# Kernel tuning notes

Hardware: AMD Instinct MI355X
Metric: run time of the kernel (lower is better)

The kernel has to match this reference:

```python
import jax, jax.numpy as jnp
import numpy as np

N, E = 5000, 10000          # nodes, edges
F_IN, F_EDGE = 16, 4        # raw node / edge feature dims
H, EH, HID3 = 96, 16, 32    # node hidden, edge hidden, edge-MLP hidden
T, L, C = 5, 10, 3          # Chebyshev order, num DeepGCN layers, num classes
LN_EPS = 1e-5


def setup_inputs() -> dict:
    key = jax.random.key(0)
    ks = jax.random.split(key, 12)
    x = jax.random.normal(ks[0], (N, F_IN), jnp.float32)
    edge_index = jax.random.randint(ks[1], (2, E), 0, N)
    ea = jax.random.uniform(ks[2], (E, F_EDGE), dtype=jnp.float32)
    # first column is an edge-type flag; ~half the edges are 'sequence' edges (type 0)
    etype = jax.random.randint(ks[3], (E,), 0, 2).astype(jnp.float32)
    edge_attr = ea.at[:, 0].set(etype)

    def glorot(k, sh, fan):
        return jax.random.normal(k, sh, jnp.float32) / np.float32(np.sqrt(fan))

    cheb_w = glorot(ks[4], (T, F_IN, H), F_IN)
    cheb_b = jnp.zeros((H,), jnp.float32)
    enc_w = glorot(ks[5], (F_EDGE, EH), F_EDGE)
    enc_b = jnp.zeros((EH,), jnp.float32)
    # per-layer NNConv edge MLP (MapE2NxN): 16 -> 32 -> 96*96
    mlp_w1 = glorot(ks[6], (L, EH, HID3), EH)
    mlp_b1 = jnp.zeros((L, HID3), jnp.float32)
    mlp_w2 = glorot(ks[7], (L, HID3, H * H), HID3) * 0.1  # keep edge-weight magnitudes sane
    mlp_b2 = jnp.zeros((L, H * H), jnp.float32)
    root = glorot(ks[8], (L, H, H), H)
    conv_b = jnp.zeros((L, H), jnp.float32)
    ln_g = jnp.ones((L, H), jnp.float32)
    ln_b = jnp.zeros((L, H), jnp.float32)
    lin_w = glorot(ks[9], (H, C), H)
    lin_b = jnp.zeros((C,), jnp.float32)
    return dict(x=x, edge_index=edge_index, edge_attr=edge_attr,
                cheb_w=cheb_w, cheb_b=cheb_b, enc_w=enc_w, enc_b=enc_b,
                mlp_w1=mlp_w1, mlp_b1=mlp_b1, mlp_w2=mlp_w2, mlp_b2=mlp_b2,
                root=root, conv_b=conv_b, ln_g=ln_g, ln_b=ln_b,
                lin_w=lin_w, lin_b=lin_b)


def _layer_norm(v, g, b):
    mu = jnp.mean(v, axis=-1, keepdims=True)
    var = jnp.mean((v - mu) ** 2, axis=-1, keepdims=True)
    return (v - mu) * jax.lax.rsqrt(var + LN_EPS) * g + b


def _cheb_conv(x, row, col, mask, W, b):
    # symmetric-normalized Laplacian, lambda_max=2 => L_hat = -D^-1/2 A D^-1/2 (diag 0)
    # mask zeroes out non-sequence edges and self loops (PyG removes self loops)
    deg = jax.ops.segment_sum(mask, row, num_segments=N)
    dinv = jnp.where(deg > 0, deg ** -0.5, 0.0)
    w = -dinv[row] * dinv[col] * mask  # [E]
    Lmul = lambda v: jax.ops.segment_sum(w[:, None] * v[row], col, num_segments=N)
    Tx0 = x
    out = Tx0 @ W[0]
    Tx1 = Lmul(x)
    out = out + Tx1 @ W[1]
    for k in range(2, T):
        Tx2 = 2.0 * Lmul(Tx1) - Tx0
        out = out + Tx2 @ W[k]
        Tx0, Tx1 = Tx1, Tx2
    return out + b


def _nnconv(x, row, col, ea, w1, b1, w2, b2, rt, cb):
    # per-edge weight matrix from edge MLP (dropout in eval mode = identity)
    We = ((ea @ w1 + b1) @ w2 + b2).reshape(E, H, H)
    msg = jnp.einsum('eh,eho->eo', x[row], We)          # gather + per-edge GEMM
    agg = jax.ops.segment_sum(msg, col, num_segments=N)  # scatter-add aggregation
    return agg + x @ rt + cb


def reference(x, edge_index, edge_attr, cheb_w, cheb_b, enc_w, enc_b,
              mlp_w1, mlp_b1, mlp_w2, mlp_b2, root, conv_b, ln_g, ln_b,
              lin_w, lin_b):
    row, col = edge_index[0], edge_index[1]
    # sequence edges (edge type 0), excluding self loops, expressed as a weight mask
    seq_mask = ((edge_attr[:, 0] == 0) & (row != col)).astype(x.dtype)
    h = _cheb_conv(x, row, col, seq_mask, cheb_w, cheb_b)          # node encoder
    ea = edge_attr @ enc_w + enc_b                                  # edge encoder
    # layer 0: conv only
    h = _nnconv(h, row, col, ea, mlp_w1[0], mlp_b1[0], mlp_w2[0], mlp_b2[0],
                root[0], conv_b[0])
    # layers 1..L-1: res+ block (norm -> relu -> [dropout=id] -> conv -> +res)
    for i in range(1, L):
        r = h
        v = jax.nn.relu(_layer_norm(h, ln_g[i], ln_b[i]))
        h = _nnconv(v, row, col, ea, mlp_w1[i], mlp_b1[i], mlp_w2[i], mlp_b2[i],
                    root[i], conv_b[i]) + r
    h = jax.nn.relu(_layer_norm(h, ln_g[0], ln_b[0]))  # layers[0].act(layers[0].norm(x))
    return h @ lin_w + lin_b
```

## Files before the change

### kernel.cpp

```cpp
#include <hip/hip_runtime.h>

#define NN 5000
#define EE 10000
#define F_IN 16
#define F_EDGE 4
#define H 96
#define EHD 16
#define HID3 32
#define T_CHEB 5
#define L_LAYERS 10
#define C_OUT 3
#define LN_EPSF 1e-5f
#define KW 576
#define MD 32
#define BM2 16
#define NBT2 313
#define KC_N 36
#define FRAG_PER_LAYER (6 * KC_N * 64)

typedef float float4v __attribute__((ext_vector_type(4)));
typedef _Float16 half2v __attribute__((ext_vector_type(2)));
typedef _Float16 half4v __attribute__((ext_vector_type(4)));
typedef _Float16 half8v __attribute__((ext_vector_type(8)));

#define MFMA16(a, b, c) __builtin_amdgcn_mfma_f32_16x16x16f16((a), (b), (c), 0, 0, 0)

__global__ void k_front(const float* __restrict__ enc_w, const float* __restrict__ enc_b,
                        const float* __restrict__ w1, const float* __restrict__ b1,
                        const float* __restrict__ w2, const float* __restrict__ b2,
                        const float* __restrict__ root,
                        const int* __restrict__ row, const int* __restrict__ col,
                        const float* __restrict__ eattr,
                        _Float16* __restrict__ Mf, float* __restrict__ deg,
                        int* __restrict__ cnt, int* __restrict__ ell_r,
                        float* __restrict__ ell_m, float4* __restrict__ ell_ea) {
    const int tid = blockIdx.x * blockDim.x + threadIdx.x;
    const int NTH = gridDim.x * blockDim.x;
    for (int idx = tid; idx < L_LAYERS * H * H; idx += NTH) {
        int i = idx / (H * H);
        int m = idx % (H * H);
        int h = m / H, o = m % H;
        const float* w2i = w2 + (size_t)i * HID3 * H * H;
        const float* w1i = w1 + i * EHD * HID3;
        float hcol[HID3];
        #pragma unroll
        for (int k2 = 0; k2 < HID3; ++k2) hcol[k2] = w2i[(size_t)k2 * H * H + m];
        float tcol[EHD];
        #pragma unroll
        for (int ke = 0; ke < EHD; ++ke) {
            float s = 0.f;
            #pragma unroll
            for (int k2 = 0; k2 < HID3; ++k2) s += w1i[ke * HID3 + k2] * hcol[k2];
            tcol[ke] = s;
        }
        float vals[6];
        #pragma unroll
        for (int f = 0; f < F_EDGE; ++f) {
            float s = 0.f;
            #pragma unroll
            for (int ke = 0; ke < EHD; ++ke) s += enc_w[f * EHD + ke] * tcol[ke];
            vals[f] = s;
        }
        float c = b2[(size_t)i * H * H + m];
        #pragma unroll
        for (int ke = 0; ke < EHD; ++ke) c += enc_b[ke] * tcol[ke];
        #pragma unroll
        for (int k2 = 0; k2 < HID3; ++k2) c += b1[i * HID3 + k2] * hcol[k2];
        vals[4] = c;
        vals[5] = root[(size_t)i * H * H + m];
        int nt = o >> 4, n15 = o & 15;
        #pragma unroll
        for (int f = 0; f < 6; ++f) {
            int K = f * 96 + h;
            int kc = K >> 4, g2 = (K & 15) >> 2, e2 = K & 3;
            int lane = n15 + 16 * g2;
            Mf[((((size_t)i * 6 + nt) * KC_N + kc) * 64 + lane) * 4 + e2] = (_Float16)vals[f];
        }
    }
    for (int e = tid; e < EE; e += NTH) {
        int r = row[e], c = col[e];
        float4 ea = *(const float4*)(eattr + e * F_EDGE);
        float m = (ea.x == 0.f && r != c) ? 1.f : 0.f;
        if (m != 0.f) atomicAdd(&deg[r], 1.f);
        int slot = atomicAdd(&cnt[c], 1);
        int p = c * MD + slot;
        ell_r[p] = r;
        ell_m[p] = m;
        ell_ea[p] = ea;
    }
}

__global__ void k_chebA(const int* __restrict__ cnt, const int* __restrict__ ell_r,
                        const float* __restrict__ ell_m, const float* __restrict__ deg,
                        const float* __restrict__ x,
                        float* __restrict__ T1, float* __restrict__ T2) {
    int t = blockIdx.x * blockDim.x + threadIdx.x;
    if (t >= NN * 4) return;
    int c = t >> 2, q = t & 3;
    float dc = deg[c];
    float dinvC = dc > 0.f ? rsqrtf(dc) : 0.f;
    int nc = cnt[c];
    const int* rp = ell_r + c * MD;
    const float* mp = ell_m + c * MD;
    float4 acc1 = make_float4(0.f, 0.f, 0.f, 0.f);
    float4 acc2 = make_float4(0.f, 0.f, 0.f, 0.f);
    for (int p = 0; p < nc; ++p) {
        if (mp[p] == 0.f) continue;
        int r = rp[p];
        float dinvR = rsqrtf(deg[r]);
        float4 xr = *(const float4*)(x + (size_t)r * F_IN + q * 4);
        acc1.x = fmaf(dinvR, xr.x, acc1.x); acc1.y = fmaf(dinvR, xr.y, acc1.y);
        acc1.z = fmaf(dinvR, xr.z, acc1.z); acc1.w = fmaf(dinvR, xr.w, acc1.w);
        float4 a = make_float4(0.f, 0.f, 0.f, 0.f);
        int nr = cnt[r];
        const int* rp2 = ell_r + r * MD;
        const float* mp2 = ell_m + r * MD;
        for (int p2 = 0; p2 < nr; ++p2) {
            if (mp2[p2] == 0.f) continue;
            int r2 = rp2[p2];
            float w2v = rsqrtf(deg[r2]);
            float4 x2 = *(const float4*)(x + (size_t)r2 * F_IN + q * 4);
            a.x = fmaf(w2v, x2.x, a.x); a.y = fmaf(w2v, x2.y, a.y);
            a.z = fmaf(w2v, x2.z, a.z); a.w = fmaf(w2v, x2.w, a.w);
        }
        float f1 = -dinvR;
        acc2.x = fmaf(dinvR, f1 * a.x, acc2.x); acc2.y = fmaf(dinvR, f1 * a.y, acc2.y);
        acc2.z = fmaf(dinvR, f1 * a.z, acc2.z); acc2.w = fmaf(dinvR, f1 * a.w, acc2.w);
    }
    float4 xc = *(const float4*)(x + (size_t)c * F_IN + q * 4);
    float f = -dinvC;
    *(float4*)(T1 + (size_t)c * F_IN + q * 4) =
        make_float4(f * acc1.x, f * acc1.y, f * acc1.z, f * acc1.w);
    float f2 = -2.f * dinvC;
    *(float4*)(T2 + (size_t)c * F_IN + q * 4) =
        make_float4(f2 * acc2.x - xc.x, f2 * acc2.y - xc.y,
                    f2 * acc2.z - xc.z, f2 * acc2.w - xc.w);
}

__global__ __launch_bounds__(256) void k_chebB(
        const int* __restrict__ cnt, const int* __restrict__ ell_r,
        const float* __restrict__ ell_m, const float* __restrict__ deg,
        const float* __restrict__ x, const float* __restrict__ T1,
        const float* __restrict__ T2, const float* __restrict__ cheb_w,
        const float* __restrict__ cheb_b, _Float16* __restrict__ vout) {
    __shared__ float wlds[T_CHEB * F_IN][H];
    __shared__ float t34[2][64][F_IN];
    const int n0 = blockIdx.x * 64;
    const int t = threadIdx.x;
    for (int i = t; i < T_CHEB * F_IN * H / 4; i += 256)
        ((float4*)wlds)[i] = ((const float4*)cheb_w)[i];
    {
        int c = n0 + (t >> 2), q = t & 3;
        if (c < NN) {
            float dc = deg[c];
            float dinvC = dc > 0.f ? rsqrtf(dc) : 0.f;
            int nc = cnt[c];
            const int* rp = ell_r + c * MD;
            const float* mp = ell_m + c * MD;
            float4 a3 = make_float4(0.f, 0.f, 0.f, 0.f);
            float4 a4 = make_float4(0.f, 0.f, 0.f, 0.f);
            for (int p = 0; p < nc; ++p) {
                if (mp[p] == 0.f) continue;
                int r = rp[p];
                float dinvR = rsqrtf(deg[r]);
                float4 t2r = *(const float4*)(T2 + (size_t)r * F_IN + q * 4);
                a3.x = fmaf(dinvR, t2r.x, a3.x); a3.y = fmaf(dinvR, t2r.y, a3.y);
                a3.z = fmaf(dinvR, t2r.z, a3.z); a3.w = fmaf(dinvR, t2r.w, a3.w);
                float4 b = make_float4(0.f, 0.f, 0.f, 0.f);
                int nr = cnt[r];
                const int* rp2 = ell_r + r * MD;
                const float* mp2 = ell_m + r * MD;
                for (int p2 = 0; p2 < nr; ++p2) {
                    if (mp2[p2] == 0.f) continue;
                    int r2 = rp2[p2];
                    float w2v = rsqrtf(deg[r2]);
                    float4 t2b = *(const float4*)(T2 + (size_t)r2 * F_IN + q * 4);
                    b.x = fmaf(w2v, t2b.x, b.x); b.y = fmaf(w2v, t2b.y, b.y);
                    b.z = fmaf(w2v, t2b.z, b.z); b.w = fmaf(w2v, t2b.w, b.w);
                }
                float fr = -2.f * dinvR;
                float4 t1r = *(const float4*)(T1 + (size_t)r * F_IN + q * 4);
                float4 t3r = make_float4(fr * b.x - t1r.x, fr * b.y - t1r.y,
                                         fr * b.z - t1r.z, fr * b.w - t1r.w);
                a4.x = fmaf(dinvR, t3r.x, a4.x); a4.y = fmaf(dinvR, t3r.y, a4.y);
                a4.z = fmaf(dinvR, t3r.z, a4.z); a4.w = fmaf(dinvR, t3r.w, a4.w);
            }
            float f3 = -2.f * dinvC;
            float4 t1c = *(const float4*)(T1 + (size_t)c * F_IN + q * 4);
            float4 t2c = *(const float4*)(T2 + (size_t)c * F_IN + q * 4);
            int lr = t >> 2;
            *(float4*)&t34[0][lr][q * 4] =
                make_float4(f3 * a3.x - t1c.x, f3 * a3.y - t1c.y,
                            f3 * a3.z - t1c.z, f3 * a3.w - t1c.w);
            *(float4*)&t34[1][lr][q * 4] =
                make_float4(f3 * a4.x - t2c.x, f3 * a4.y - t2c.y,
                            f3 * a4.z - t2c.z, f3 * a4.w - t2c.w);
        }
    }
    __syncthreads();
    {
        int lr = t >> 2, n = n0 + lr, cseg = t & 3;
        if (n >= NN) return;
        float txv[T_CHEB * F_IN];
        #pragma unroll
        for (int q = 0; q < 4; ++q) {
            *(float4*)(txv + q * 4)      = *(const float4*)(x  + (size_t)n * F_IN + q * 4);
            *(float4*)(txv + 16 + q * 4) = *(const float4*)(T1 + (size_t)n * F_IN + q * 4);
            *(float4*)(txv + 32 + q * 4) = *(const float4*)(T2 + (size_t)n * F_IN + q * 4);
            *(float4*)(txv + 48 + q * 4) = *(const float4*)&t34[0][lr][q * 4];
            *(float4*)(txv + 64 + q * 4) = *(const float4*)&t34[1][lr][q * 4];
        }
        _Float16* vr = vout + (size_t)n * H + cseg * 24;
        #pragma unroll 4
        for (int c = 0; c < 24; ++c) {
            int o = cseg * 24 + c;
            float s = cheb_b[o];
            #pragma unroll
            for (int kf = 0; kf < T_CHEB * F_IN; ++kf)
                s = fmaf(txv[kf], wlds[kf][o], s);
            vr[c] = (_Float16)s;
        }
    }
}

__global__ __launch_bounds__(512) void k_layer(
        const _Float16* __restrict__ vcur, const float* __restrict__ hres,
        const int* __restrict__ cnt, const int* __restrict__ ell_r,
        const float4* __restrict__ ell_ea, const _Float16* __restrict__ MfL,
        const float* __restrict__ cb, const float* __restrict__ lg,
        const float* __restrict__ lb, const float* __restrict__ lin_w,
        const float* __restrict__ lin_b,
        float* __restrict__ hnext, _Float16* __restrict__ vnext,
        float* __restrict__ outp, int isLast) {
    __shared__ __align__(16) _Float16 zs[BM2][584];
    __shared__ float hop[4][BM2][100];
    const int n0 = blockIdx.x * BM2;
    const int t = threadIdx.x;

    if (t < 256) {
        int r = t >> 4, lane16 = t & 15;
        int gn = n0 + r, c0 = lane16 * 6;
        float accf[5][6] = {};
        half2v self0 = (half2v)(_Float16)0.f, self1 = self0, self2 = self0;
        if (gn < NN) {
            const _Float16* sv = vcur + (size_t)gn * H + c0;
            self0 = *(const half2v*)(sv + 0);
            self1 = *(const half2v*)(sv + 2);
            self2 = *(const half2v*)(sv + 4);
            int nc = cnt[gn];
            const int* rp = ell_r + gn * MD;
            const float4* eap = ell_ea + gn * MD;
            for (int p = 0; p < nc; ++p) {
                int r2 = rp[p];
                float4 ea = eap[p];
                const _Float16* vv = vcur + (size_t)r2 * H + c0;
                half2v v0 = *(const half2v*)(vv + 0);
                half2v v1 = *(const half2v*)(vv + 2);
                half2v v2 = *(const half2v*)(vv + 4);
                float vf[6] = {(float)v0[0], (float)v0[1], (float)v1[0],
                               (float)v1[1], (float)v2[0], (float)v2[1]};
                const float cf[4] = {ea.x, ea.y, ea.z, ea.w};
                #pragma unroll
                for (int f = 0; f < 4; ++f)
                    #pragma unroll
                    for (int j = 0; j < 6; ++j)
                        accf[f][j] = fmaf(cf[f], vf[j], accf[f][j]);
                #pragma unroll
                for (int j = 0; j < 6; ++j) accf[4][j] += vf[j];
            }
        }
        #pragma unroll
        for (int f = 0; f < 5; ++f) {
            _Float16* zp = &zs[r][f * 96 + c0];
            *(half2v*)(zp + 0) = half2v{(_Float16)accf[f][0], (_Float16)accf[f][1]};
            *(half2v*)(zp + 2) = half2v{(_Float16)accf[f][2], (_Float16)accf[f][3]};
            *(half2v*)(zp + 4) = half2v{(_Float16)accf[f][4], (_Float16)accf[f][5]};
        }
        _Float16* zp = &zs[r][480 + c0];
        *(half2v*)(zp + 0) = self0;
        *(half2v*)(zp + 2) = self1;
        *(half2v*)(zp + 4) = self2;
    }
    __syncthreads();

    {
        const int wid = t >> 6, l = t & 63;
        const int n15 = l & 15, g = l >> 4;
        const int ntBase = (wid & 1) * 3;
        const int kSeg = wid >> 1;
        const int kcBase = kSeg * 9;
        const half4v* Mf4 = (const half4v*)MfL;
        half4v af[9];
        #pragma unroll
        for (int kk = 0; kk < 9; ++kk)
            af[kk] = *(const half4v*)&zs[n15][(kcBase + kk) * 16 + 4 * g];
        float4v acc3[3] = {};
        #pragma unroll
        for (int j = 0; j < 3; ++j) {
            int nt = ntBase + j;
            const half4v* Bp = Mf4 + ((size_t)nt * KC_N + kcBase) * 64 + l;
            #pragma unroll
            for (int kk = 0; kk < 9; ++kk)
                acc3[j] = MFMA16(af[kk], Bp[kk * 64], acc3[j]);
        }
        #pragma unroll
        for (int j = 0; j < 3; ++j) {
            int cc = (ntBase + j) * 16 + n15;
            #pragma unroll
            for (int e = 0; e < 4; ++e)
                hop[kSeg][4 * g + e][cc] = acc3[j][e];
        }
    }
    __syncthreads();

    if (t < 256) {
        int r = t >> 4, lane16 = t & 15;
        int gn = n0 + r, c0 = lane16 * 6;
        float hv[6];
        #pragma unroll
        for (int j = 0; j < 6; ++j)
            hv[j] = hop[0][r][c0 + j] + hop[1][r][c0 + j]
                  + hop[2][r][c0 + j] + hop[3][r][c0 + j] + cb[c0 + j];
        if (hres && gn < NN) {
            const float* rp = hres + (size_t)gn * H + c0;
            #pragma unroll
            for (int j = 0; j < 6; j += 2) {
                float2 rv = *(const float2*)(rp + j);
                hv[j] += rv.x; hv[j + 1] += rv.y;
            }
        }
        if (!isLast && gn < NN) {
            float* hp = hnext + (size_t)gn * H + c0;
            #pragma unroll
            for (int j = 0; j < 6; j += 2)
                *(float2*)(hp + j) = make_float2(hv[j], hv[j + 1]);
        }
        float s = 0.f;
        #pragma unroll
        for (int j = 0; j < 6; ++j) s += hv[j];
        s += __shfl_xor(s, 1); s += __shfl_xor(s, 2);
        s += __shfl_xor(s, 4); s += __shfl_xor(s, 8);
        float mu = s * (1.0f / H);
        float vvr = 0.f;
        #pragma unroll
        for (int j = 0; j < 6; ++j) { float d = hv[j] - mu; vvr += d * d; }
        vvr += __shfl_xor(vvr, 1); vvr += __shfl_xor(vvr, 2);
        vvr += __shfl_xor(vvr, 4); vvr += __shfl_xor(vvr, 8);
        float is = rsqrtf(vvr * (1.0f / H) + LN_EPSF);
        const float* gp = lg + c0;
        const float* bp = lb + c0;
        float yv[6];
        #pragma unroll
        for (int j = 0; j < 6; ++j)
            yv[j] = fmaxf(fmaf((hv[j] - mu) * is, gp[j], bp[j]), 0.f);
        if (!isLast) {
            if (gn < NN) {
                _Float16* vp = vnext + (size_t)gn * H + c0;
                *(half2v*)(vp + 0) = half2v{(_Float16)yv[0], (_Float16)yv[1]};
                *(half2v*)(vp + 2) = half2v{(_Float16)yv[2], (_Float16)yv[3]};
                *(half2v*)(vp + 4) = half2v{(_Float16)yv[4], (_Float16)yv[5]};
            }
        } else {
            float a0 = 0.f, a1 = 0.f, a2 = 0.f;
            #pragma unroll
            for (int j = 0; j < 6; ++j) {
                int oo = c0 + j;
                a0 = fmaf(yv[j], lin_w[oo * C_OUT + 0], a0);
                a1 = fmaf(yv[j], lin_w[oo * C_OUT + 1], a1);
                a2 = fmaf(yv[j], lin_w[oo * C_OUT + 2], a2);
            }
            a0 += __shfl_xor(a0, 1); a0 += __shfl_xor(a0, 2);
            a0 += __shfl_xor(a0, 4); a0 += __shfl_xor(a0, 8);
            a1 += __shfl_xor(a1, 1); a1 += __shfl_xor(a1, 2);
            a1 += __shfl_xor(a1, 4); a1 += __shfl_xor(a1, 8);
            a2 += __shfl_xor(a2, 1); a2 += __shfl_xor(a2, 2);
            a2 += __shfl_xor(a2, 4); a2 += __shfl_xor(a2, 8);
            if (lane16 == 0 && gn < NN) {
                outp[gn * C_OUT + 0] = a0 + lin_b[0];
                outp[gn * C_OUT + 1] = a1 + lin_b[1];
                outp[gn * C_OUT + 2] = a2 + lin_b[2];
            }
        }
    }
}

extern "C" void kernel_launch(void* const* d_in, const int* in_sizes, int n_in,
                              void* d_out, int out_size, void* d_ws, size_t ws_size,
                              hipStream_t stream) {
    const float* x      = (const float*)d_in[0];
    const int*   row    = (const int*)d_in[1];
    const int*   col    = (const int*)d_in[1] + EE;
    const float* eattr  = (const float*)d_in[2];
    const float* cheb_w = (const float*)d_in[3];
    const float* cheb_b = (const float*)d_in[4];
    const float* enc_w  = (const float*)d_in[5];
    const float* enc_b  = (const float*)d_in[6];
    const float* w1     = (const float*)d_in[7];
    const float* b1     = (const float*)d_in[8];
    const float* w2     = (const float*)d_in[9];
    const float* b2     = (const float*)d_in[10];
    const float* root   = (const float*)d_in[11];
    const float* conv_b = (const float*)d_in[12];
    const float* ln_g   = (const float*)d_in[13];
    const float* ln_b   = (const float*)d_in[14];
    const float* lin_w  = (const float*)d_in[15];
    const float* lin_b  = (const float*)d_in[16];

    char* base = (char*)d_ws;
    size_t off = 0;
    auto alloc = [&](size_t nbytes) {
        char* p = base + off;
        off += (nbytes + 255) / 256 * 256;
        return p;
    };
    float*    deg    = (float*)alloc(NN * 4);
    int*      cnt    = (int*)  alloc(NN * 4);
    size_t    ctl_bytes = off;
    _Float16* Mfrag  = (_Float16*)alloc((size_t)L_LAYERS * FRAG_PER_LAYER * 4 * 2);
    float*    T1     = (float*)alloc((size_t)NN * F_IN * 4);
    float*    T2     = (float*)alloc((size_t)NN * F_IN * 4);
    int*      ell_r  = (int*)  alloc((size_t)NN * MD * 4);
    float*    ell_m  = (float*)alloc((size_t)NN * MD * 4);
    float4*   ell_ea = (float4*)alloc((size_t)NN * MD * 16);
    _Float16* v0     = (_Float16*)alloc((size_t)NN * H * 2);
    _Float16* v1     = (_Float16*)alloc((size_t)NN * H * 2);
    float*    hA     = (float*)alloc((size_t)NN * H * 4);
    float*    hB     = (float*)alloc((size_t)NN * H * 4);
    (void)ws_size; (void)n_in; (void)in_sizes; (void)out_size;

    const int B = 256;
    auto G = [](long n, int b) { return (int)((n + b - 1) / b); };

    (void)hipMemsetAsync(deg, 0, ctl_bytes, stream);
    k_front<<<360, B, 0, stream>>>(enc_w, enc_b, w1, b1, w2, b2, root,
                                   row, col, eattr, Mfrag, deg, cnt, ell_r, ell_m, ell_ea);
    k_chebA<<<G((long)NN * 4, B), B, 0, stream>>>(cnt, ell_r, ell_m, deg, x, T1, T2);
    k_chebB<<<G(NN, 64), B, 0, stream>>>(cnt, ell_r, ell_m, deg, x, T1, T2,
                                         cheb_w, cheb_b, v0);

    _Float16* vbuf[2] = { v0, v1 };
    float*    hbuf[2] = { hA, hB };
    for (int li = 0; li < L_LAYERS; ++li) {
        int isLast = (li == L_LAYERS - 1);
        const _Float16* vcur = vbuf[li & 1];
        _Float16*       vnx  = vbuf[(li + 1) & 1];
        const float*    hres = (li > 0) ? hbuf[(li + 1) & 1] : nullptr;
        float*          hnx  = hbuf[li & 1];
        const float* elg = isLast ? ln_g : ln_g + (li + 1) * H;
        const float* elb = isLast ? ln_b : ln_b + (li + 1) * H;
        k_layer<<<NBT2, 512, 0, stream>>>(
            vcur, hres, cnt, ell_r, ell_ea,
            Mfrag + (size_t)li * FRAG_PER_LAYER * 4,
            conv_b + li * H, elg, elb, lin_w, lin_b,
            hnx, vnx, (float*)d_out, isLast);
    }
}
```

Baseline: 164.6 us.

## Build edge ELL in one block with LDS atomics; prefetch MFMA B fragments early

Edge bucketing and degree counting now run in a dedicated extra block of k_front using shared-memory atomics, and the block writes deg and cnt directly. This removes the separate hipMemsetAsync and the global atomics. In k_layer, each wave loads its B-operand weight fragments into registers at kernel start, so those global loads overlap the neighbor-gather phase instead of sitting behind the barrier. The costs are one block serially handling all 10000 edges, which may lengthen the front kernel, and 27 extra half4 registers per thread in k_layer, which may reduce occupancy.

```diff
diff --git a/kernel.cpp b/kernel.cpp
--- a/kernel.cpp
+++ b/kernel.cpp
@@ -25,17 +25,41 @@
 
 #define MFMA16(a, b, c) __builtin_amdgcn_mfma_f32_16x16x16f16((a), (b), (c), 0, 0, 0)
 
-__global__ void k_front(const float* __restrict__ enc_w, const float* __restrict__ enc_b,
-                        const float* __restrict__ w1, const float* __restrict__ b1,
-                        const float* __restrict__ w2, const float* __restrict__ b2,
-                        const float* __restrict__ root,
-                        const int* __restrict__ row, const int* __restrict__ col,
-                        const float* __restrict__ eattr,
-                        _Float16* __restrict__ Mf, float* __restrict__ deg,
-                        int* __restrict__ cnt, int* __restrict__ ell_r,
-                        float* __restrict__ ell_m, float4* __restrict__ ell_ea) {
-    const int tid = blockIdx.x * blockDim.x + threadIdx.x;
-    const int NTH = gridDim.x * blockDim.x;
+__global__ __launch_bounds__(256) void k_front(
+        const float* __restrict__ enc_w, const float* __restrict__ enc_b,
+        const float* __restrict__ w1, const float* __restrict__ b1,
+        const float* __restrict__ w2, const float* __restrict__ b2,
+        const float* __restrict__ root,
+        const int* __restrict__ row, const int* __restrict__ col,
+        const float* __restrict__ eattr,
+        _Float16* __restrict__ Mf, float* __restrict__ deg,
+        int* __restrict__ cnt, int* __restrict__ ell_r,
+        float* __restrict__ ell_m, float4* __restrict__ ell_ea) {
+    __shared__ int sdeg[NN];
+    __shared__ int scnt[NN];
+    if (blockIdx.x == 0) {
+        for (int i = threadIdx.x; i < NN; i += 256) { sdeg[i] = 0; scnt[i] = 0; }
+        __syncthreads();
+        for (int e = threadIdx.x; e < EE; e += 256) {
+            int r = row[e], c = col[e];
+            float4 ea = *(const float4*)(eattr + e * F_EDGE);
+            float m = (ea.x == 0.f && r != c) ? 1.f : 0.f;
+            if (m != 0.f) atomicAdd(&sdeg[r], 1);
+            int slot = atomicAdd(&scnt[c], 1);
+            int p = c * MD + slot;
+            ell_r[p] = r;
+            ell_m[p] = m;
+            ell_ea[p] = ea;
+        }
+        __syncthreads();
+        for (int i = threadIdx.x; i < NN; i += 256) {
+            deg[i] = (float)sdeg[i];
+            cnt[i] = scnt[i];
+        }
+        return;
+    }
+    const int tid = (blockIdx.x - 1) * 256 + threadIdx.x;
+    const int NTH = (gridDim.x - 1) * 256;
     for (int idx = tid; idx < L_LAYERS * H * H; idx += NTH) {
         int i = idx / (H * H);
         int m = idx % (H * H);
@@ -76,17 +100,6 @@
             int lane = n15 + 16 * g2;
             Mf[((((size_t)i * 6 + nt) * KC_N + kc) * 64 + lane) * 4 + e2] = (_Float16)vals[f];
         }
-    }
-    for (int e = tid; e < EE; e += NTH) {
-        int r = row[e], c = col[e];
-        float4 ea = *(const float4*)(eattr + e * F_EDGE);
-        float m = (ea.x == 0.f && r != c) ? 1.f : 0.f;
-        if (m != 0.f) atomicAdd(&deg[r], 1.f);
-        int slot = atomicAdd(&cnt[c], 1);
-        int p = c * MD + slot;
-        ell_r[p] = r;
-        ell_m[p] = m;
-        ell_ea[p] = ea;
     }
 }
 
@@ -237,6 +250,20 @@
     const int n0 = blockIdx.x * BM2;
     const int t = threadIdx.x;
 
+    const int wid = t >> 6, l = t & 63;
+    const int n15 = l & 15, g = l >> 4;
+    const int ntBase = (wid & 1) * 3;
+    const int kSeg = wid >> 1;
+    const int kcBase = kSeg * 9;
+    const half4v* Mf4 = (const half4v*)MfL;
+    half4v bfr[3][9];
+    #pragma unroll
+    for (int j = 0; j < 3; ++j) {
+        const half4v* Bp = Mf4 + ((size_t)(ntBase + j) * KC_N + kcBase) * 64 + l;
+        #pragma unroll
+        for (int kk = 0; kk < 9; ++kk) bfr[j][kk] = Bp[kk * 64];
+    }
+
     if (t < 256) {
         int r = t >> 4, lane16 = t & 15;
         int gn = n0 + r, c0 = lane16 * 6;
@@ -284,25 +311,16 @@
     __syncthreads();
 
     {
-        const int wid = t >> 6, l = t & 63;
-        const int n15 = l & 15, g = l >> 4;
-        const int ntBase = (wid & 1) * 3;
-        const int kSeg = wid >> 1;
-        const int kcBase = kSeg * 9;
-        const half4v* Mf4 = (const half4v*)MfL;
         half4v af[9];
         #pragma unroll
         for (int kk = 0; kk < 9; ++kk)
             af[kk] = *(const half4v*)&zs[n15][(kcBase + kk) * 16 + 4 * g];
         float4v acc3[3] = {};
         #pragma unroll
-        for (int j = 0; j < 3; ++j) {
-            int nt = ntBase + j;
-            const half4v* Bp = Mf4 + ((size_t)nt * KC_N + kcBase) * 64 + l;
+        for (int j = 0; j < 3; ++j)
             #pragma unroll
             for (int kk = 0; kk < 9; ++kk)
-                acc3[j] = MFMA16(af[kk], Bp[kk * 64], acc3[j]);
-        }
+                acc3[j] = MFMA16(af[kk], bfr[j][kk], acc3[j]);
         #pragma unroll
         for (int j = 0; j < 3; ++j) {
             int cc = (ntBase + j) * 16 + n15;
@@ -415,7 +433,6 @@
     };
     float*    deg    = (float*)alloc(NN * 4);
     int*      cnt    = (int*)  alloc(NN * 4);
-    size_t    ctl_bytes = off;
     _Float16* Mfrag  = (_Float16*)alloc((size_t)L_LAYERS * FRAG_PER_LAYER * 4 * 2);
     float*    T1     = (float*)alloc((size_t)NN * F_IN * 4);
     float*    T2     = (float*)alloc((size_t)NN * F_IN * 4);
@@ -431,8 +448,7 @@
     const int B = 256;
     auto G = [](long n, int b) { return (int)((n + b - 1) / b); };
 
-    (void)hipMemsetAsync(deg, 0, ctl_bytes, stream);
-    k_front<<<360, B, 0, stream>>>(enc_w, enc_b, w1, b1, w2, b2, root,
+    k_front<<<361, B, 0, stream>>>(enc_w, enc_b, w1, b1, w2, b2, root,
                                    row, col, eattr, Mfrag, deg, cnt, ell_r, ell_m, ell_ea);
     k_chebA<<<G((long)NN * 4, B), B, 0, stream>>>(cnt, ell_r, ell_m, deg, x, T1, T2);
     k_chebB<<<G(NN, 64), B, 0, stream>>>(cnt, ell_r, ell_m, deg, x, T1, T2,
```

After: 183.2 us. 11.3% more time.
